# Kernel tuning notes

Hardware: AMD Instinct MI355X
Metric: run time of the kernel (lower is better)

The kernel has to match this reference:

```python
import jax, jax.numpy as jnp
import numpy as np
from jax import lax

K = 8        # num neighbors (excluding self)
ALPHA = 0.5
EPS = 1e-12


def setup_inputs() -> dict:
    key = jax.random.key(0)
    k1, k2 = jax.random.split(key)
    B, N = 4, 4096
    pred = jax.random.normal(k1, (B, N, 3), dtype=jnp.float32)
    target = jax.random.normal(k2, (B, N, 3), dtype=jnp.float32)
    return {"pred": pred, "target": target}


def _pdist(x):
    # x: [B, N, 3] -> Euclidean distance matrix [B, N, N]
    sq = jnp.sum(x * x, axis=-1)                                # [B, N]
    d2 = sq[:, :, None] + sq[:, None, :] - 2.0 * jnp.einsum('bnd,bmd->bnm', x, x)
    return jnp.sqrt(jnp.maximum(d2, EPS))


def _knn_idx(dist, k):
    # smallest k+1 distances, drop self (first column)
    _, idx = lax.top_k(-dist, k + 1)                            # [B, N, k+1]
    return idx[:, :, 1:]                                        # [B, N, k]


def _gather_points(pts, idx):
    # pts: [B, N, 3], idx: [B, N, k] -> [B, N, k, 3]
    return jax.vmap(lambda p, i: p[i])(pts, idx)


def reference(pred, target):
    # Per-batch losses are means over equal-size point sets, so averaging over
    # (B, N) jointly is identical to the original per-batch loop + /B.
    pred_dist = _pdist(pred)
    target_dist = _pdist(target)
    pred_idx = _knn_idx(pred_dist, K)
    target_idx = _knn_idx(target_dist, K)

    # density: mean kNN distance per point
    pred_density = jnp.mean(jnp.take_along_axis(pred_dist, pred_idx, axis=2), axis=2)
    target_density = jnp.mean(jnp.take_along_axis(target_dist, target_idx, axis=2), axis=2)
    density_loss = jnp.mean((pred_density - target_density) ** 2)

    # direction similarity of normalized neighbor offsets
    pred_nb = _gather_points(pred, pred_idx)                    # [B, N, K, 3]
    target_nb = _gather_points(target, target_idx)
    pred_vec = pred_nb - pred[:, :, None, :]
    target_vec = target_nb - target[:, :, None, :]
    pn = pred_vec / jnp.maximum(jnp.linalg.norm(pred_vec, axis=-1, keepdims=True), EPS)
    tn = target_vec / jnp.maximum(jnp.linalg.norm(target_vec, axis=-1, keepdims=True), EPS)
    direction_loss = 1.0 - jnp.mean(jnp.sum(pn * tn, axis=-1))

    # local covariance (curvature proxy)
    pred_cov = jnp.einsum('bnki,bnkj->bnij', pred_vec, pred_vec) / K    # [B, N, 3, 3]
    target_cov = jnp.einsum('bnki,bnkj->bnij', target_vec, target_vec) / K
    cov_diff = jnp.sqrt(jnp.sum((pred_cov - target_cov) ** 2, axis=(-2, -1)))
    curvature_loss = jnp.mean(cov_diff)

    return density_loss + ALPHA * direction_loss + (1.0 - ALPHA) * curvature_loss
```

## Files before the change

kernel.cpp:

```cpp
#include <hip/hip_runtime.h>
#include <cstdint>
#include <cstddef>

#define NPTS   4096
#define BATCH  4
#define KNN    8
#define NC     16
#define CHN    (NPTS / NC)
#define PD     4
#define SD     3
#define EPS_F  1e-12f

__device__ __forceinline__ uint32_t u32min(uint32_t a, uint32_t b) { return a < b ? a : b; }
__device__ __forceinline__ uint32_t u32max(uint32_t a, uint32_t b) { return a > b ? a : b; }

__device__ __forceinline__ uint32_t umed3(uint32_t a, uint32_t b, uint32_t c) {
  uint32_t d;
  asm("v_med3_u32 %0, %1, %2, %3" : "=v"(d) : "v"(a), "v"(b), "v"(c));
  return d;
}

template <int D>
__device__ __forceinline__ void insertD(uint32_t (&loc)[D], uint32_t key) {
  uint32_t prev = loc[0];
  loc[0] = u32min(prev, key);
#pragma unroll
  for (int m = 1; m < D; ++m) {
    const uint32_t cur = loc[m];
    loc[m] = umed3(prev, cur, key);
    prev = cur;
  }
}

template <int D>
__device__ __forceinline__ void scan_chunk(const float4* __restrict__ c4, int j0,
                                           float xix, float xiy, float xiz,
                                           uint32_t (&loc)[D]) {
#pragma unroll
  for (int k = 0; k < D; ++k) loc[k] = 0xFFFFFFFFu;
#pragma unroll 4
  for (int t4 = 0; t4 < CHN / 4; ++t4) {
    const float4 q0 = c4[3 * t4 + 0];
    const float4 q1 = c4[3 * t4 + 1];
    const float4 q2 = c4[3 * t4 + 2];
    const uint32_t jb = (uint32_t)(j0 + 4 * t4);
    {
      const float dx = xix - q0.x, dy = xiy - q0.y, dz = xiz - q0.z;
      const float d2 = fmaf(dx, dx, fmaf(dy, dy, dz * dz));
      insertD<D>(loc, (__float_as_uint(d2) & 0xFFFFF000u) | (jb + 0u));
    }
    {
      const float dx = xix - q0.w, dy = xiy - q1.x, dz = xiz - q1.y;
      const float d2 = fmaf(dx, dx, fmaf(dy, dy, dz * dz));
      insertD<D>(loc, (__float_as_uint(d2) & 0xFFFFF000u) | (jb + 1u));
    }
    {
      const float dx = xix - q1.z, dy = xiy - q1.w, dz = xiz - q2.x;
      const float d2 = fmaf(dx, dx, fmaf(dy, dy, dz * dz));
      insertD<D>(loc, (__float_as_uint(d2) & 0xFFFFF000u) | (jb + 2u));
    }
    {
      const float dx = xix - q2.y, dy = xiy - q2.z, dz = xiz - q2.w;
      const float d2 = fmaf(dx, dx, fmaf(dy, dy, dz * dz));
      insertD<D>(loc, (__float_as_uint(d2) & 0xFFFFF000u) | (jb + 3u));
    }
  }
}

__global__ void __launch_bounds__(256, 4)
knn_partial_k(const float* __restrict__ pred, const float* __restrict__ tgt,
              uint32_t* __restrict__ partial, double* __restrict__ acc,
              uint32_t* __restrict__ ticket) {
  if (blockIdx.x == 0 && threadIdx.x == 0) {
    acc[0] = 0.0; acc[1] = 0.0; acc[2] = 0.0;
    *ticket = 0u;
  }

  int bx = blockIdx.x;
  const int chunk = bx & (NC - 1); bx /= NC;
  const int ig    = bx & 15; bx >>= 4;
  const int b     = bx & 3;  bx >>= 2;
  const int cloud = bx;

  const float* __restrict__ pts = (cloud ? tgt : pred) + (size_t)b * NPTS * 3;
  const int tid = threadIdx.x;
  const int i = ig * 256 + tid;
  const int j0 = chunk * CHN;

  const float xix = pts[3 * i + 0];
  const float xiy = pts[3 * i + 1];
  const float xiz = pts[3 * i + 2];

  const float4* __restrict__ c4 = (const float4*)(pts + 3 * j0);

  uint4 o;
  if (ig == chunk) {
    uint32_t loc[SD + 1];
    scan_chunk<SD + 1>(c4, j0, xix, xiy, xiz, loc);
    o = make_uint4(loc[1], loc[2], loc[3], 0xFFFFFFFFu);
  } else {
    uint32_t loc[SD];
    scan_chunk<SD>(c4, j0, xix, xiy, xiz, loc);
    o = make_uint4(loc[0], loc[1], loc[2], 0xFFFFFFFFu);
  }
  uint32_t* p = partial +
      ((((size_t)(cloud * BATCH + b) * NC + chunk) * NPTS) + (size_t)i) * PD;
  *(uint4*)p = o;
}

__device__ __forceinline__ void merge2(uint32_t A[KNN], const uint32_t B[KNN]) {
  uint32_t t[KNN];
#pragma unroll
  for (int m = 0; m < KNN; ++m) t[m] = u32min(A[m], B[KNN - 1 - m]);
#define CEU(x, y) { uint32_t lo = u32min(t[x], t[y]); uint32_t hi = u32max(t[x], t[y]); t[x] = lo; t[y] = hi; }
  CEU(0,4) CEU(1,5) CEU(2,6) CEU(3,7)
  CEU(0,2) CEU(1,3) CEU(4,6) CEU(5,7)
  CEU(0,1) CEU(2,3) CEU(4,5) CEU(6,7)
#undef CEU
#pragma unroll
  for (int m = 0; m < KNN; ++m) A[m] = t[m];
}

__device__ __forceinline__ void merge44(const uint2 a0, const uint2 a1,
                                        const uint2 b0, const uint2 b1,
                                        uint32_t s[KNN]) {
  s[0] = a0.x; s[1] = a0.y; s[2] = a1.x; s[3] = a1.y;
  s[4] = b1.y; s[5] = b1.x; s[6] = b0.y; s[7] = b0.x;
#define CEU(x, y) { uint32_t lo = u32min(s[x], s[y]); uint32_t hi = u32max(s[x], s[y]); s[x] = lo; s[y] = hi; }
  CEU(0,4) CEU(1,5) CEU(2,6) CEU(3,7)
  CEU(0,2) CEU(1,3) CEU(4,6) CEU(5,7)
  CEU(0,1) CEU(2,3) CEU(4,5) CEU(6,7)
#undef CEU
}

__device__ __forceinline__ void merge_all(const uint32_t* __restrict__ base,
                                          int i, uint32_t v[KNN]) {
  const size_t stride = (size_t)NPTS * PD;
  const uint32_t* p = base + (size_t)i * PD;
  uint2 q[NC][2];
#pragma unroll
  for (int c = 0; c < NC; ++c) {
    q[c][0] = *(const uint2*)(p + (size_t)c * stride);
    q[c][1] = *(const uint2*)(p + (size_t)c * stride + 2);
  }
  uint32_t L[NC / 2][KNN];
#pragma unroll
  for (int c = 0; c < NC / 2; ++c)
    merge44(q[2 * c][0], q[2 * c][1], q[2 * c + 1][0], q[2 * c + 1][1], L[c]);
  merge2(L[0], L[1]); merge2(L[2], L[3]); merge2(L[4], L[5]); merge2(L[6], L[7]);
  merge2(L[0], L[2]); merge2(L[4], L[6]);
  merge2(L[0], L[4]);
#pragma unroll
  for (int m = 0; m < KNN; ++m) v[m] = L[0][m];
}

__device__ __forceinline__ void cloud_stats(const float* __restrict__ C, int i,
                                            const uint32_t v[KNN],
                                            float& dsum, float cov[6],
                                            float nx[KNN], float ny[KNN], float nz[KNN]) {
  const float qx = C[3 * i], qy = C[3 * i + 1], qz = C[3 * i + 2];
  float jx[KNN], jy[KNN], jz[KNN];
#pragma unroll
  for (int k = 0; k < KNN; ++k) {
    const int j = (int)(v[k] & 0xFFFu);
    jx[k] = C[3 * j]; jy[k] = C[3 * j + 1]; jz[k] = C[3 * j + 2];
  }
  dsum = 0.f;
#pragma unroll
  for (int m = 0; m < 6; ++m) cov[m] = 0.f;
#pragma unroll
  for (int k = 0; k < KNN; ++k) {
    const float ax = jx[k] - qx, ay = jy[k] - qy, az = jz[k] - qz;
    const float d2 = fmaf(ax, ax, fmaf(ay, ay, az * az));
    const float dist = sqrtf(fmaxf(d2, EPS_F));
    const float inv = 1.0f / fmaxf(dist, EPS_F);
    dsum += dist;
    cov[0] += ax * ax; cov[1] += ay * ay; cov[2] += az * az;
    cov[3] += ax * ay; cov[4] += ax * az; cov[5] += ay * az;
    nx[k] = ax * inv; ny[k] = ay * inv; nz[k] = az * inv;
  }
}

__global__ void __launch_bounds__(64, 1)
loss_k(const float* __restrict__ pred, const float* __restrict__ tgt,
       const uint32_t* __restrict__ partial, double* __restrict__ acc,
       uint32_t* __restrict__ ticket, float* __restrict__ out) {
  const int p = blockIdx.x * 64 + threadIdx.x;
  const int b = p >> 12;
  const int i = p & (NPTS - 1);

  const float* __restrict__ P = pred + (size_t)b * NPTS * 3;
  const float* __restrict__ T = tgt  + (size_t)b * NPTS * 3;

  const size_t cstride = (size_t)NC * NPTS * PD;
  uint32_t vp[KNN], vt[KNN];
  merge_all(partial + (size_t)(0 * BATCH + b) * cstride, i, vp);
  merge_all(partial + (size_t)(1 * BATCH + b) * cstride, i, vt);

  float dsp, dst, pcov[6], tcov[6];
  float pnx[KNN], pny[KNN], pnz[KNN], tnx[KNN], tny[KNN], tnz[KNN];
  cloud_stats(P, i, vp, dsp, pcov, pnx, pny, pnz);
  cloud_stats(T, i, vt, dst, tcov, tnx, tny, tnz);

  float sdot = 0.f;
#pragma unroll
  for (int k = 0; k < KNN; ++k)
    sdot += pnx[k] * tnx[k] + pny[k] * tny[k] + pnz[k] * tnz[k];

  const float densp = dsp * (1.0f / KNN);
  const float denst = dst * (1.0f / KNN);
  float e = (densp - denst) * (densp - denst);

  const float dxx = (pcov[0] - tcov[0]) * (1.0f / KNN);
  const float dyy = (pcov[1] - tcov[1]) * (1.0f / KNN);
  const float dzz = (pcov[2] - tcov[2]) * (1.0f / KNN);
  const float dxy = (pcov[3] - tcov[3]) * (1.0f / KNN);
  const float dxz = (pcov[4] - tcov[4]) * (1.0f / KNN);
  const float dyz = (pcov[5] - tcov[5]) * (1.0f / KNN);
  float cfro = sqrtf(dxx * dxx + dyy * dyy + dzz * dzz
                     + 2.0f * (dxy * dxy + dxz * dxz + dyz * dyz));
  float s = sdot;

#pragma unroll
  for (int off = 32; off > 0; off >>= 1) {
    e    += __shfl_down(e, off);
    s    += __shfl_down(s, off);
    cfro += __shfl_down(cfro, off);
  }
  if (threadIdx.x == 0) {
    atomicAdd(&acc[0], (double)e);
    atomicAdd(&acc[1], (double)s);
    atomicAdd(&acc[2], (double)cfro);
    __threadfence();
    const unsigned rank = atomicAdd(ticket, 1u) + 1u;
    if (rank == (unsigned)((BATCH * NPTS) / 64)) {
      __threadfence();
      const double ee = __hip_atomic_load(&acc[0], __ATOMIC_RELAXED, __HIP_MEMORY_SCOPE_AGENT);
      const double ss = __hip_atomic_load(&acc[1], __ATOMIC_RELAXED, __HIP_MEMORY_SCOPE_AGENT);
      const double cc = __hip_atomic_load(&acc[2], __ATOMIC_RELAXED, __HIP_MEMORY_SCOPE_AGENT);
      const double BN = (double)BATCH * (double)NPTS;
      out[0] = (float)(ee / BN + 0.5 * (1.0 - ss / (BN * (double)KNN)) + 0.5 * (cc / BN));
    }
  }
}

extern "C" void kernel_launch(void* const* d_in, const int* in_sizes, int n_in,
                              void* d_out, int out_size, void* d_ws, size_t ws_size,
                              hipStream_t stream) {
  const float* pred = (const float*)d_in[0];
  const float* tgt  = (const float*)d_in[1];
  double* acc = (double*)d_ws;
  uint32_t* ticket = (uint32_t*)((char*)d_ws + 64);
  uint32_t* partial = (uint32_t*)((char*)d_ws + 4096);

  knn_partial_k<<<2 * BATCH * (NPTS / 256) * NC, 256, 0, stream>>>(
      pred, tgt, partial, acc, ticket);
  loss_k<<<(BATCH * NPTS) / 64, 64, 0, stream>>>(
      pred, tgt, partial, acc, ticket, (float*)d_out);
}
```

Baseline: 104.5 us.

## Stage candidate chunk in LDS and replace atomic accumulation with per-block partial sums

The kNN partial kernel now copies each block's 256-point candidate chunk into shared memory once and scans it from LDS instead of issuing global float4 loads per thread. The unroll factor drops and the launch-bounds occupancy hint is raised, trading per-thread ILP for more resident waves. The loss kernel writes per-block partial sums to a workspace array and the last-arriving block reduces them, replacing three contended double-precision atomics per block. This also makes the final sum deterministic, at the cost of an extra reduction pass inside a single block.

```diff
diff --git a/kernel.cpp b/kernel.cpp
--- a/kernel.cpp
+++ b/kernel.cpp
@@ -10,6 +10,7 @@
 #define PD     4
 #define SD     3
 #define EPS_F  1e-12f
+#define NBLK2  ((BATCH * NPTS) / 64)
 
 __device__ __forceinline__ uint32_t u32min(uint32_t a, uint32_t b) { return a < b ? a : b; }
 __device__ __forceinline__ uint32_t u32max(uint32_t a, uint32_t b) { return a > b ? a : b; }
@@ -38,7 +39,7 @@
                                            uint32_t (&loc)[D]) {
 #pragma unroll
   for (int k = 0; k < D; ++k) loc[k] = 0xFFFFFFFFu;
-#pragma unroll 4
+#pragma unroll 2
   for (int t4 = 0; t4 < CHN / 4; ++t4) {
     const float4 q0 = c4[3 * t4 + 0];
     const float4 q1 = c4[3 * t4 + 1];
@@ -67,14 +68,12 @@
   }
 }
 
-__global__ void __launch_bounds__(256, 4)
+__global__ void __launch_bounds__(256, 8)
 knn_partial_k(const float* __restrict__ pred, const float* __restrict__ tgt,
-              uint32_t* __restrict__ partial, double* __restrict__ acc,
-              uint32_t* __restrict__ ticket) {
-  if (blockIdx.x == 0 && threadIdx.x == 0) {
-    acc[0] = 0.0; acc[1] = 0.0; acc[2] = 0.0;
-    *ticket = 0u;
-  }
+              uint32_t* __restrict__ partial, uint32_t* __restrict__ ticket) {
+  if (blockIdx.x == 0 && threadIdx.x == 0) *ticket = 0u;
+
+  __shared__ float4 lds4[3 * CHN / 4];
 
   int bx = blockIdx.x;
   const int chunk = bx & (NC - 1); bx /= NC;
@@ -87,12 +86,15 @@
   const int i = ig * 256 + tid;
   const int j0 = chunk * CHN;
 
+  const float4* __restrict__ g4 = (const float4*)(pts + 3 * j0);
+  if (tid < 3 * CHN / 4) lds4[tid] = g4[tid];
+
   const float xix = pts[3 * i + 0];
   const float xiy = pts[3 * i + 1];
   const float xiz = pts[3 * i + 2];
-
-  const float4* __restrict__ c4 = (const float4*)(pts + 3 * j0);
-
+  __syncthreads();
+
+  const float4* c4 = lds4;
   uint4 o;
   if (ig == chunk) {
     uint32_t loc[SD + 1];
@@ -183,7 +185,7 @@
 
 __global__ void __launch_bounds__(64, 1)
 loss_k(const float* __restrict__ pred, const float* __restrict__ tgt,
-       const uint32_t* __restrict__ partial, double* __restrict__ acc,
+       const uint32_t* __restrict__ partial, double* __restrict__ bsum,
        uint32_t* __restrict__ ticket, float* __restrict__ out) {
   const int p = blockIdx.x * 64 + threadIdx.x;
   const int b = p >> 12;
@@ -227,17 +229,32 @@
     s    += __shfl_down(s, off);
     cfro += __shfl_down(cfro, off);
   }
+
+  unsigned rank = 0u;
   if (threadIdx.x == 0) {
-    atomicAdd(&acc[0], (double)e);
-    atomicAdd(&acc[1], (double)s);
-    atomicAdd(&acc[2], (double)cfro);
+    double* d = bsum + 3 * (size_t)blockIdx.x;
+    d[0] = (double)e; d[1] = (double)s; d[2] = (double)cfro;
     __threadfence();
-    const unsigned rank = atomicAdd(ticket, 1u) + 1u;
-    if (rank == (unsigned)((BATCH * NPTS) / 64)) {
-      __threadfence();
-      const double ee = __hip_atomic_load(&acc[0], __ATOMIC_RELAXED, __HIP_MEMORY_SCOPE_AGENT);
-      const double ss = __hip_atomic_load(&acc[1], __ATOMIC_RELAXED, __HIP_MEMORY_SCOPE_AGENT);
-      const double cc = __hip_atomic_load(&acc[2], __ATOMIC_RELAXED, __HIP_MEMORY_SCOPE_AGENT);
+    rank = atomicAdd(ticket, 1u) + 1u;
+  }
+  rank = __shfl(rank, 0);
+  if (rank == (unsigned)NBLK2) {
+    __threadfence();
+    double ee = 0.0, ss = 0.0, cc = 0.0;
+#pragma unroll
+    for (int g = 0; g < NBLK2 / 64; ++g) {
+      double* d = bsum + 3 * (size_t)(threadIdx.x + 64 * g);
+      ee += __hip_atomic_load(&d[0], __ATOMIC_RELAXED, __HIP_MEMORY_SCOPE_AGENT);
+      ss += __hip_atomic_load(&d[1], __ATOMIC_RELAXED, __HIP_MEMORY_SCOPE_AGENT);
+      cc += __hip_atomic_load(&d[2], __ATOMIC_RELAXED, __HIP_MEMORY_SCOPE_AGENT);
+    }
+#pragma unroll
+    for (int off = 32; off > 0; off >>= 1) {
+      ee += __shfl_down(ee, off);
+      ss += __shfl_down(ss, off);
+      cc += __shfl_down(cc, off);
+    }
+    if (threadIdx.x == 0) {
       const double BN = (double)BATCH * (double)NPTS;
       out[0] = (float)(ee / BN + 0.5 * (1.0 - ss / (BN * (double)KNN)) + 0.5 * (cc / BN));
     }
@@ -249,12 +266,12 @@
                               hipStream_t stream) {
   const float* pred = (const float*)d_in[0];
   const float* tgt  = (const float*)d_in[1];
-  double* acc = (double*)d_ws;
-  uint32_t* ticket = (uint32_t*)((char*)d_ws + 64);
-  uint32_t* partial = (uint32_t*)((char*)d_ws + 4096);
+  uint32_t* ticket  = (uint32_t*)((char*)d_ws + 64);
+  double*   bsum    = (double*)((char*)d_ws + 4096);
+  uint32_t* partial = (uint32_t*)((char*)d_ws + 65536);
 
   knn_partial_k<<<2 * BATCH * (NPTS / 256) * NC, 256, 0, stream>>>(
-      pred, tgt, partial, acc, ticket);
-  loss_k<<<(BATCH * NPTS) / 64, 64, 0, stream>>>(
-      pred, tgt, partial, acc, ticket, (float*)d_out);
-}
+      pred, tgt, partial, ticket);
+  loss_k<<<NBLK2, 64, 0, stream>>>(
+      pred, tgt, partial, bsum, ticket, (float*)d_out);
+}
```

Result: faster. 97.04 us (-7.1%).
